# Performance work log

Measured on AMD Instinct MI355X. Metric: run time of the kernel, lower is better.

Reference implementation:

```python
import jax, jax.numpy as jnp
import numpy as np

N, E, D, EDIM = 50000, 800000, 128, 1
LN_EPS = 1e-5
NORM_FACTOR = 1.0


def _ln(x, g, b):
    m = jnp.mean(x, axis=-1, keepdims=True)
    v = jnp.var(x, axis=-1, keepdims=True)
    return (x - m) * jax.lax.rsqrt(v + LN_EPS) * g + b


def _mlp(x, w1, b1, g, be, w2, b2):
    # Linear -> SiLU -> LayerNorm -> Linear (matches nn.Sequential in msg_net/out_net)
    h = jax.nn.silu(x @ w1 + b1)
    h = _ln(h, g, be)
    return h @ w2 + b2


def setup_inputs() -> dict:
    key = jax.random.key(0)
    ks = jax.random.split(key, 24)
    s = 1.0 / np.sqrt(D)
    sa = 1.0 / np.sqrt(2 * D + EDIM)
    f32 = jnp.float32
    return {
        "h": jax.random.normal(ks[0], (N, D), f32),
        "edge_attr": jax.random.uniform(ks[1], (E, EDIM), f32),
        "row": jax.random.randint(ks[2], (E,), 0, N),
        "col": jax.random.randint(ks[3], (E,), 0, N),
        "node_mask": jnp.ones((N, 1), f32),
        "edge_mask": jnp.ones((E, 1), f32),
        "lin_w": jax.random.normal(ks[4], (D, D), f32) * s,
        "lin_b": jnp.zeros((D,), f32),
        "msg_w1": jax.random.normal(ks[5], (D, D), f32) * s,
        "msg_b1": jnp.zeros((D,), f32),
        "msg_ln_g": jnp.ones((D,), f32),
        "msg_ln_b": jnp.zeros((D,), f32),
        "msg_w2": jax.random.normal(ks[6], (D, D), f32) * s,
        "msg_b2": jnp.zeros((D,), f32),
        "att_w1": jax.random.normal(ks[7], (2 * D + EDIM, D), f32) * sa,
        "att_b1": jnp.zeros((D,), f32),
        "att_w2": jax.random.normal(ks[8], (D, 1), f32) * s,
        "att_b2": jnp.zeros((1,), f32),
        "out_w1": jax.random.normal(ks[9], (D, D), f32) * s,
        "out_b1": jnp.zeros((D,), f32),
        "out_ln_g": jnp.ones((D,), f32),
        "out_ln_b": jnp.zeros((D,), f32),
        "out_w2": jax.random.normal(ks[10], (D, D), f32) * s,
        "out_b2": jnp.zeros((D,), f32),
        "ln_g": jnp.ones((D,), f32),
        "ln_b": jnp.zeros((D,), f32),
    }


def reference(h, edge_attr, row, col, node_mask, edge_mask,
              lin_w, lin_b,
              msg_w1, msg_b1, msg_ln_g, msg_ln_b, msg_w2, msg_b2,
              att_w1, att_b1, att_w2, att_b2,
              out_w1, out_b1, out_ln_g, out_ln_b, out_w2, out_b2,
              ln_g, ln_b):
    # h = self.linear(h)
    x = h @ lin_w + lin_b                                    # [N, D]
    # msg_net transform of node features
    x_ = _mlp(x, msg_w1, msg_b1, msg_ln_g, msg_ln_b, msg_w2, msg_b2)
    # DenseAtt: cat(x[row], x[col], edge_attr) -> MLP -> sigmoid -> * edge_mask
    feat = jnp.concatenate([x[row], x[col], edge_attr], axis=1)   # [E, 2D+edge_dim]
    att = jax.nn.sigmoid(jax.nn.silu(feat @ att_w1 + att_b1) @ att_w2 + att_b2)
    att = att * edge_mask                                    # [E, 1]
    # gather -> weighted message -> scatter_add (unsorted_segment_sum, 'sum' norm)
    msg = jax.ops.segment_sum(x_[col] * att, row, num_segments=N) / NORM_FACTOR
    # out_net transform, residual, final LayerNorm
    msg = _mlp(msg, out_w1, out_b1, out_ln_g, out_ln_b, out_w2, out_b2)
    return _ln(x + msg, ln_g, ln_b)                          # [N, D]
```

## Files before the change

kernel.cpp:

```cpp
#include <hip/hip_runtime.h>

#define LN_EPS 1e-5f

typedef __attribute__((ext_vector_type(8))) short short8;
typedef __attribute__((ext_vector_type(4))) float f32x4;

__device__ __forceinline__ float sigf(float x) {
    return __builtin_amdgcn_rcpf(1.0f + __expf(-x));
}

__device__ __forceinline__ unsigned short f2bf(float f) {
    unsigned u = __float_as_uint(f);
    return (unsigned short)((u + 0x7fffu + ((u >> 16) & 1u)) >> 16);
}
__device__ __forceinline__ unsigned f2bf2(float lo, float hi) {
    return (unsigned)f2bf(lo) | ((unsigned)f2bf(hi) << 16);
}
__device__ __forceinline__ void bf2f(unsigned u, float& lo, float& hi) {
    lo = __uint_as_float(u << 16);
    hi = __uint_as_float(u & 0xffff0000u);
}
__device__ __forceinline__ void bf8f(uint4 p, float* o) {
    bf2f(p.x, o[0], o[1]); bf2f(p.y, o[2], o[3]);
    bf2f(p.z, o[4], o[5]); bf2f(p.w, o[6], o[7]);
}
__device__ __forceinline__ float bf1f(unsigned short s) {
    return __uint_as_float(((unsigned)s) << 16);
}

__device__ __forceinline__ float quad_add_all(float x) {
    int v = __builtin_amdgcn_update_dpp(0, __float_as_int(x), 0xB1, 0xF, 0xF, true);
    x += __int_as_float(v);
    v = __builtin_amdgcn_update_dpp(0, __float_as_int(x), 0x4E, 0xF, 0xF, true);
    x += __int_as_float(v);
    return x;
}

__global__ __launch_bounds__(256)
void prep_w(const float* __restrict__ lin_w, const float* __restrict__ msg_w1,
            const float* __restrict__ msg_w2, const float* __restrict__ att_w1,
            const float* __restrict__ out_w1, const float* __restrict__ out_w2,
            const float* __restrict__ att_b1, unsigned short* __restrict__ wp,
            float* __restrict__ bias256)
{
    const int idx = blockIdx.x * 256 + threadIdx.x;
    if (idx < 8 * 16384) {
        const int m = idx >> 14, r = idx & 16383;
        const int k = r >> 7, n = r & 127;
        const float* src; int slot; int fnBase = 0;
        switch (m) {
            case 0: src = lin_w;  slot = 0; break;
            case 1: src = msg_w1; slot = 1; break;
            case 2: src = msg_w2; slot = 2; break;
            case 3: src = att_w1; slot = 3; break;
            case 4: src = att_w1 + 128 * 128; slot = 3; fnBase = 8; break;
            case 5: src = out_w1; slot = 5; break;
            default: src = out_w2; slot = 6; break;
        }
        const float v = src[k * 128 + n];
        const int fn = fnBase + (n >> 4);
        const int fk = k >> 5, kb = (k >> 3) & 3, j = k & 7;
        const size_t dst = (size_t)slot * 16384 + ((size_t)((fn * 4 + fk) * 64 + (n & 15) + 16 * kb)) * 8 + j;
        wp[dst] = f2bf(v);
    } else if (idx < 8 * 16384 + 256) {
        const int t = idx - 8 * 16384;
        bias256[t] = (t < 128) ? att_b1[t] : 0.f;
    }
}

__device__ __forceinline__ short8 ldA_bf(const unsigned short* A, size_t row, int k0) {
    return *(const short8*)(A + row * 128 + k0);
}
__device__ __forceinline__ short8 ldA_f32(const float* A, size_t row, int k0) {
    const float* ap = A + row * 128 + k0;
    const float4 f0 = *(const float4*)ap;
    const float4 f1 = *(const float4*)(ap + 4);
    union { unsigned u[4]; short8 s; } v;
    v.u[0] = f2bf2(f0.x, f0.y); v.u[1] = f2bf2(f0.z, f0.w);
    v.u[2] = f2bf2(f1.x, f1.y); v.u[3] = f2bf2(f1.z, f1.w);
    return v.s;
}

template<int NFN, int ABF, int SPLIT>
__global__ __launch_bounds__(256, NFN == 8 ? 4 : 3)
void gemm_mfma(const void* __restrict__ Av, const unsigned short* __restrict__ Wp,
               const float* __restrict__ bias,
               unsigned short* __restrict__ C1, int ld1,
               unsigned short* __restrict__ C2, int ld2, int nrows)
{
    const int tid = threadIdx.x;
    const int w = tid >> 6, lane = tid & 63;
    const int r0 = blockIdx.x * 64;
    const int arow = r0 + w * 16 + (lane & 15);
    const size_t rowc = (arow < nrows) ? (size_t)arow : (size_t)(nrows - 1);
    const int kh = (lane >> 4) * 8;

    short8 a[4];
#pragma unroll
    for (int fk = 0; fk < 4; ++fk)
        a[fk] = ABF ? ldA_bf((const unsigned short*)Av, rowc, fk * 32 + kh)
                    : ldA_f32((const float*)Av, rowc, fk * 32 + kh);

    const short8* Bf = (const short8*)Wp;
    f32x4 acc[NFN];
#pragma unroll
    for (int fn = 0; fn < NFN; ++fn) acc[fn] = (f32x4){0.f, 0.f, 0.f, 0.f};
#pragma unroll
    for (int fk = 0; fk < 4; ++fk)
#pragma unroll
        for (int fn = 0; fn < NFN; ++fn)
            acc[fn] = __builtin_amdgcn_mfma_f32_16x16x32_bf16(a[fk], Bf[(fn * 4 + fk) * 64 + lane], acc[fn], 0, 0, 0);

    const int cn = lane & 15, rq = lane >> 4;
    float bv[NFN];
#pragma unroll
    for (int fn = 0; fn < NFN; ++fn) bv[fn] = bias ? bias[fn * 16 + cn] : 0.f;

#pragma unroll
    for (int reg = 0; reg < 4; ++reg) {
        const int gr = r0 + w * 16 + rq * 4 + reg;
        if (gr < nrows) {
#pragma unroll
            for (int fn = 0; fn < NFN; ++fn) {
                const float v = acc[fn][reg] + bv[fn];
                if (SPLIT) {
                    if (fn < 8) C1[(size_t)gr * ld1 + fn * 16 + cn] = f2bf(v);
                    else        C2[(size_t)gr * ld2 + (fn - 8) * 16 + cn] = f2bf(v);
                } else {
                    C1[(size_t)gr * ld1 + fn * 16 + cn] = f2bf(v);
                }
            }
        }
    }
}

template<int EPI2>
__global__ __launch_bounds__(256, 4)
void gemm2_mfma(const unsigned short* __restrict__ Av,
                const unsigned short* __restrict__ Wp1, const float* __restrict__ b1,
                const float* __restrict__ ln1g, const float* __restrict__ ln1b,
                const unsigned short* __restrict__ Wp2, const float* __restrict__ b2,
                const float* __restrict__ ln2g, const float* __restrict__ ln2b,
                const unsigned short* __restrict__ resH, void* __restrict__ Cv, int nrows)
{
    __shared__ unsigned short hof[4 * 2048];
    const int tid = threadIdx.x;
    const int w = tid >> 6, lane = tid & 63;
    const int r0 = blockIdx.x * 64;
    const int arow = r0 + w * 16 + (lane & 15);
    const size_t rowc = (arow < nrows) ? (size_t)arow : (size_t)(nrows - 1);
    const int kh = (lane >> 4) * 8;
    const int cn = lane & 15, rq = lane >> 4;

    short8 a[4];
#pragma unroll
    for (int fk = 0; fk < 4; ++fk)
        a[fk] = ldA_bf(Av, rowc, fk * 32 + kh);

    const short8* B1f = (const short8*)Wp1;
    f32x4 acc[8];
#pragma unroll
    for (int fn = 0; fn < 8; ++fn) acc[fn] = (f32x4){0.f, 0.f, 0.f, 0.f};
#pragma unroll
    for (int fk = 0; fk < 4; ++fk)
#pragma unroll
        for (int fn = 0; fn < 8; ++fn)
            acc[fn] = __builtin_amdgcn_mfma_f32_16x16x32_bf16(a[fk], B1f[(fn * 4 + fk) * 64 + lane], acc[fn], 0, 0, 0);

    unsigned short* hw = hof + w * 2048;
    {
        float bv[8], gv[8], bbv[8];
#pragma unroll
        for (int fn = 0; fn < 8; ++fn) {
            bv[fn] = b1[fn * 16 + cn]; gv[fn] = ln1g[fn * 16 + cn]; bbv[fn] = ln1b[fn * 16 + cn];
        }
#pragma unroll
        for (int reg = 0; reg < 4; ++reg) {
            float val[8];
            float sum = 0.f, sq = 0.f;
#pragma unroll
            for (int fn = 0; fn < 8; ++fn) {
                float v = acc[fn][reg] + bv[fn];
                v = v * sigf(v);
                val[fn] = v; sum += v; sq += v * v;
            }
#pragma unroll
            for (int m = 1; m < 16; m <<= 1) { sum += __shfl_xor(sum, m); sq += __shfl_xor(sq, m); }
            const float mean = sum * (1.f / 128.f);
            const float var = sq * (1.f / 128.f) - mean * mean;
            const float rstd = rsqrtf(var + LN_EPS);
            const int row16 = rq * 4 + reg;
            const int sw = (row16 & 7) << 3;
#pragma unroll
            for (int fn = 0; fn < 8; ++fn) {
                const float o = (val[fn] - mean) * rstd * gv[fn] + bbv[fn];
                hw[row16 * 128 + ((fn * 16 + cn) ^ sw)] = f2bf(o);
            }
        }
    }

    short8 a2[4];
    {
        const int row16 = lane & 15;
        const int sw = (row16 & 7) << 3;
#pragma unroll
        for (int fk = 0; fk < 4; ++fk)
            a2[fk] = *(const short8*)(hw + row16 * 128 + ((fk * 32 + kh) ^ sw));
    }

    const short8* B2f = (const short8*)Wp2;
    f32x4 acc2[8];
#pragma unroll
    for (int fn = 0; fn < 8; ++fn) acc2[fn] = (f32x4){0.f, 0.f, 0.f, 0.f};
#pragma unroll
    for (int fk = 0; fk < 4; ++fk)
#pragma unroll
        for (int fn = 0; fn < 8; ++fn)
            acc2[fn] = __builtin_amdgcn_mfma_f32_16x16x32_bf16(a2[fk], B2f[(fn * 4 + fk) * 64 + lane], acc2[fn], 0, 0, 0);

    float bv2[8];
#pragma unroll
    for (int fn = 0; fn < 8; ++fn) bv2[fn] = b2[fn * 16 + cn];

    if (EPI2 == 0) {
        unsigned short* Ch = (unsigned short*)Cv;
#pragma unroll
        for (int reg = 0; reg < 4; ++reg) {
            const int gr = r0 + w * 16 + rq * 4 + reg;
            if (gr < nrows) {
#pragma unroll
                for (int fn = 0; fn < 8; ++fn)
                    Ch[(size_t)gr * 128 + fn * 16 + cn] = f2bf(acc2[fn][reg] + bv2[fn]);
            }
        }
    } else {
        float* Cf = (float*)Cv;
        float gv[8], bbv[8];
#pragma unroll
        for (int fn = 0; fn < 8; ++fn) { gv[fn] = ln2g[fn * 16 + cn]; bbv[fn] = ln2b[fn * 16 + cn]; }
#pragma unroll
        for (int reg = 0; reg < 4; ++reg) {
            const int gr = r0 + w * 16 + rq * 4 + reg;
            const int grc = gr < nrows ? gr : nrows - 1;
            float val[8];
            float sum = 0.f, sq = 0.f;
#pragma unroll
            for (int fn = 0; fn < 8; ++fn) {
                float v = acc2[fn][reg] + bv2[fn] + bf1f(resH[(size_t)grc * 128 + fn * 16 + cn]);
                val[fn] = v; sum += v; sq += v * v;
            }
#pragma unroll
            for (int m = 1; m < 16; m <<= 1) { sum += __shfl_xor(sum, m); sq += __shfl_xor(sq, m); }
            const float mean = sum * (1.f / 128.f);
            const float var = sq * (1.f / 128.f) - mean * mean;
            const float rstd = rsqrtf(var + LN_EPS);
            if (gr < nrows) {
#pragma unroll
                for (int fn = 0; fn < 8; ++fn)
                    Cf[(size_t)gr * 128 + fn * 16 + cn] = (val[fn] - mean) * rstd * gv[fn] + bbv[fn];
            }
        }
    }
}


__global__ __launch_bounds__(256)
void hist_k(const int* __restrict__ row, int* __restrict__ cnt, int E)
{
    for (int e = blockIdx.x * blockDim.x + threadIdx.x; e < E; e += gridDim.x * blockDim.x)
        atomicAdd(&cnt[row[e]], 1);
}

__global__ __launch_bounds__(1024)
void scan_a(const int* __restrict__ cnt, int* __restrict__ off,
            int* __restrict__ btot, int n)
{
    __shared__ int wsum[16];
    const int tid = threadIdx.x, lane = tid & 63, wv = tid >> 6;
    const int i = blockIdx.x * 1024 + tid;
    const int v = (i < n) ? cnt[i] : 0;
    int incl = v;
#pragma unroll
    for (int d = 1; d < 64; d <<= 1) { int t = __shfl_up(incl, d); if (lane >= d) incl += t; }
    if (lane == 63) wsum[wv] = incl;
    __syncthreads();
    if (tid == 0) {
        int run = 0;
        for (int ww = 0; ww < 16; ++ww) { int t = wsum[ww]; wsum[ww] = run; run += t; }
    }
    __syncthreads();
    if (i < n) off[i] = wsum[wv] + incl - v;
    if (tid == 1023) btot[blockIdx.x] = wsum[15] + incl;
}

__global__ __launch_bounds__(64)
void scan_b(int* __restrict__ btot, int* __restrict__ bexc,
            int* __restrict__ off, int n, int nb, int E)
{
    const int t = threadIdx.x;
    const int v = (t < nb) ? btot[t] : 0;
    int incl = v;
#pragma unroll
    for (int d = 1; d < 64; d <<= 1) { int u = __shfl_up(incl, d); if (t >= d) incl += u; }
    if (t < nb) bexc[t] = incl - v;
    if (t == 0) off[n] = E;
}

__global__ __launch_bounds__(1024)
void scan_c(int* __restrict__ off, const int* __restrict__ bexc,
            int* __restrict__ cursor, int n)
{
    const int i = blockIdx.x * 1024 + threadIdx.x;
    if (i < n) {
        const int o = off[i] + bexc[blockIdx.x];
        off[i] = o;
        cursor[i] = o;
    }
}

__global__ __launch_bounds__(256)
void scatter_k(const int* __restrict__ row, const int* __restrict__ col,
               const float* __restrict__ ea, const float* __restrict__ em,
               int* __restrict__ cursor, uint4* __restrict__ erec, int E)
{
    const int tid = blockIdx.x * blockDim.x + threadIdx.x;
    const int stride = gridDim.x * blockDim.x;
    for (int e0 = tid; e0 < E; e0 += stride * 4) {
        uint4 rec[4]; int pos[4]; bool val[4];
#pragma unroll
        for (int u = 0; u < 4; ++u) {
            const int e = e0 + u * stride;
            val[u] = e < E;
            const int ec = val[u] ? e : 0;
            rec[u].x = (unsigned)row[ec];
            rec[u].y = (unsigned)col[ec];
            rec[u].z = __float_as_uint(ea[ec]);
            rec[u].w = __float_as_uint(em[ec]);
        }
#pragma unroll
        for (int u = 0; u < 4; ++u)
            if (val[u]) pos[u] = atomicAdd(&cursor[rec[u].x], 1);
#pragma unroll
        for (int u = 0; u < 4; ++u)
            if (val[u]) erec[pos[u]] = rec[u];
    }
}

__global__ __launch_bounds__(256, 4)
void att_edge(const unsigned short* __restrict__ xrH,
              const unsigned short* __restrict__ xcH,
              const uint4* __restrict__ erec, const float* __restrict__ we_,
              const float* __restrict__ w2_, const float* __restrict__ b2p,
              uint2* __restrict__ catS, int E)
{
    const int lane = threadIdx.x & 63;
    const int q = lane & 3;
    const int gwid = (blockIdx.x * blockDim.x + threadIdx.x) >> 6;
    const int nw = (gridDim.x * blockDim.x) >> 6;

    float we[32], w2[32];
#pragma unroll
    for (int ch = 0; ch < 4; ++ch) {
        const float4 a0 = ((const float4*)we_)[ch * 8 + q * 2];
        const float4 a1 = ((const float4*)we_)[ch * 8 + q * 2 + 1];
        we[ch * 8 + 0] = a0.x; we[ch * 8 + 1] = a0.y; we[ch * 8 + 2] = a0.z; we[ch * 8 + 3] = a0.w;
        we[ch * 8 + 4] = a1.x; we[ch * 8 + 5] = a1.y; we[ch * 8 + 6] = a1.z; we[ch * 8 + 7] = a1.w;
        const float4 c0 = ((const float4*)w2_)[ch * 8 + q * 2];
        const float4 c1 = ((const float4*)w2_)[ch * 8 + q * 2 + 1];
        w2[ch * 8 + 0] = c0.x; w2[ch * 8 + 1] = c0.y; w2[ch * 8 + 2] = c0.z; w2[ch * 8 + 3] = c0.w;
        w2[ch * 8 + 4] = c1.x; w2[ch * 8 + 5] = c1.y; w2[ch * 8 + 6] = c1.z; w2[ch * 8 + 7] = c1.w;
    }
    const float b2 = *b2p;

    for (int base = gwid * 16; base < E; base += nw * 16) {
        const int e = base + (lane >> 2);
        const bool valid = e < E;
        const int ec = valid ? e : E - 1;
        const uint4 rec = erec[ec];
        const int r = (int)rec.x, c = (int)rec.y;
        const float eax = __uint_as_float(rec.z);
        const float emv = __uint_as_float(rec.w);
        const unsigned short* xr = xrH + (size_t)r * 128;
        const unsigned short* xc = xcH + (size_t)c * 128;
        float p = 0.f;
#pragma unroll
        for (int ch = 0; ch < 4; ++ch) {
            const uint4 pa = *(const uint4*)(xr + ch * 32 + q * 8);
            const uint4 pb = *(const uint4*)(xc + ch * 32 + q * 8);
            float xa[8], xb[8];
            bf8f(pa, xa); bf8f(pb, xb);
#pragma unroll
            for (int i = 0; i < 8; ++i) {
                const float t = xa[i] + xb[i] + eax * we[ch * 8 + i];
                p += t * sigf(t) * w2[ch * 8 + i];
            }
        }
        p = quad_add_all(p);
        const float att = sigf(p + b2) * emv;
        if (valid && q == 0) catS[e] = make_uint2(rec.y, __float_as_uint(att));
    }
}

__global__ __launch_bounds__(256)
void accum_k(const unsigned short* __restrict__ xmH, const int* __restrict__ off,
             const uint2* __restrict__ catS, unsigned short* __restrict__ msgH, int N)
{
    const int lane = threadIdx.x & 63;
    const int g = lane >> 4, l = lane & 15;
    const int gwid = (blockIdx.x * blockDim.x + threadIdx.x) >> 6;
    const int nw = (gridDim.x * blockDim.x) >> 6;
    const uint4* xm4 = (const uint4*)xmH;

    for (int wid = gwid; wid < N; wid += nw) {
        int j0 = off[wid];
        const int jend = off[wid + 1];
        float acc[8] = {0.f, 0.f, 0.f, 0.f, 0.f, 0.f, 0.f, 0.f};

        for (; j0 + 16 <= jend; j0 += 16) {
            uint2 ca[4]; uint4 pk[4];
#pragma unroll
            for (int u = 0; u < 4; ++u) ca[u] = catS[j0 + u * 4 + g];
#pragma unroll
            for (int u = 0; u < 4; ++u) pk[u] = xm4[(size_t)ca[u].x * 16 + l];
#pragma unroll
            for (int u = 0; u < 4; ++u) {
                const float att = __uint_as_float(ca[u].y);
                float xm[8];
                bf8f(pk[u], xm);
#pragma unroll
                for (int i = 0; i < 8; ++i) acc[i] = fmaf(att, xm[i], acc[i]);
            }
        }
        for (; j0 + 8 <= jend; j0 += 8) {
            const uint2 caA = catS[j0 + g];
            const uint2 caB = catS[j0 + 4 + g];
            const uint4 pA = xm4[(size_t)caA.x * 16 + l];
            const uint4 pB = xm4[(size_t)caB.x * 16 + l];
            const float attA = __uint_as_float(caA.y);
            const float attB = __uint_as_float(caB.y);
            float xmA[8], xmB[8];
            bf8f(pA, xmA); bf8f(pB, xmB);
#pragma unroll
            for (int i = 0; i < 8; ++i)
                acc[i] = fmaf(attB, xmB[i], fmaf(attA, xmA[i], acc[i]));
        }
        for (; j0 < jend; j0 += 4) {
            const int je = j0 + g;
            const bool valid = je < jend;
            const int jc = valid ? je : jend - 1;
            const uint2 ca = catS[jc];
            const uint4 p = xm4[(size_t)ca.x * 16 + l];
            const float att = valid ? __uint_as_float(ca.y) : 0.f;
            float xm[8];
            bf8f(p, xm);
#pragma unroll
            for (int i = 0; i < 8; ++i) acc[i] = fmaf(att, xm[i], acc[i]);
        }

#pragma unroll
        for (int i = 0; i < 8; ++i) {
            acc[i] += __shfl_xor(acc[i], 16);
            acc[i] += __shfl_xor(acc[i], 32);
        }
        if (g == 0) {
            uint4 pk;
            pk.x = f2bf2(acc[0], acc[1]); pk.y = f2bf2(acc[2], acc[3]);
            pk.z = f2bf2(acc[4], acc[5]); pk.w = f2bf2(acc[6], acc[7]);
            ((uint4*)msgH)[(size_t)wid * 16 + l] = pk;
        }
    }
}

extern "C" void kernel_launch(void* const* d_in, const int* in_sizes, int n_in,
                              void* d_out, int out_size, void* d_ws, size_t ws_size,
                              hipStream_t stream)
{
    const float* h        = (const float*)d_in[0];
    const float* edge_attr= (const float*)d_in[1];
    const int*   row      = (const int*)d_in[2];
    const int*   col      = (const int*)d_in[3];
    const float* edge_mask= (const float*)d_in[5];
    const float* lin_w    = (const float*)d_in[6];
    const float* lin_b    = (const float*)d_in[7];
    const float* msg_w1   = (const float*)d_in[8];
    const float* msg_b1   = (const float*)d_in[9];
    const float* msg_ln_g = (const float*)d_in[10];
    const float* msg_ln_b = (const float*)d_in[11];
    const float* msg_w2   = (const float*)d_in[12];
    const float* msg_b2   = (const float*)d_in[13];
    const float* att_w1   = (const float*)d_in[14];
    const float* att_b1   = (const float*)d_in[15];
    const float* att_w2   = (const float*)d_in[16];
    const float* att_b2   = (const float*)d_in[17];
    const float* out_w1   = (const float*)d_in[18];
    const float* out_b1   = (const float*)d_in[19];
    const float* out_ln_g = (const float*)d_in[20];
    const float* out_ln_b = (const float*)d_in[21];
    const float* out_w2   = (const float*)d_in[22];
    const float* out_b2   = (const float*)d_in[23];
    const float* ln_g     = (const float*)d_in[24];
    const float* ln_b     = (const float*)d_in[25];

    const int N = in_sizes[0] / 128;
    const int E = in_sizes[2];
    const size_t NF = (size_t)N * 128;

    unsigned short* xbH  = (unsigned short*)d_ws;
    unsigned short* xrH  = xbH + NF;
    unsigned short* xcH  = xrH + NF;
    unsigned short* xmH  = xcH + NF;
    unsigned short* msgH = xmH + NF;
    int*    cnt   = (int*)(msgH + NF);
    int*    off   = cnt + N;
    int*    btot  = off + N + 8;
    int*    bexc  = btot + 64;
    uint4*  erec  = (uint4*)(bexc + 64 + 24);
    uint2*  catS  = (uint2*)(erec + E);
    unsigned short* wp = (unsigned short*)(catS + E);
    float* bias256 = (float*)(wp + 8 * 16384);

    const int gb = (N + 63) / 64;
    const int nb = (N + 1023) / 1024;
    const int sgrid = (E + 256 * 4 - 1) / (256 * 4);

    prep_w<<<513, 256, 0, stream>>>(lin_w, msg_w1, msg_w2, att_w1, out_w1, out_w2,
                                    att_b1, wp, bias256);
    hipMemsetAsync(cnt, 0, (size_t)N * sizeof(int), stream);
    hist_k<<<1024, 256, 0, stream>>>(row, cnt, E);
    scan_a<<<nb, 1024, 0, stream>>>(cnt, off, btot, N);
    scan_b<<<1, 64, 0, stream>>>(btot, bexc, off, N, nb, E);
    scan_c<<<nb, 1024, 0, stream>>>(off, bexc, cnt, N);
    scatter_k<<<sgrid, 256, 0, stream>>>(row, col, edge_attr, edge_mask,
                                         cnt, erec, E);

    gemm_mfma<8, 0, 0><<<gb, 256, 0, stream>>>(h, wp, lin_b, xbH, 128, nullptr, 0, N);
    gemm_mfma<16, 1, 1><<<gb, 256, 0, stream>>>(xbH, wp + 3 * 16384, bias256, xrH, 128, xcH, 128, N);
    att_edge<<<2048, 256, 0, stream>>>(xrH, xcH, erec,
                                       att_w1 + 256 * 128, att_w2, att_b2, catS, E);

    gemm2_mfma<0><<<gb, 256, 0, stream>>>(xbH, wp + 16384, msg_b1, msg_ln_g, msg_ln_b,
                                          wp + 2 * 16384, msg_b2, nullptr, nullptr,
                                          nullptr, xmH, N);

    accum_k<<<2048, 256, 0, stream>>>(xmH, off, catS, msgH, N);

    gemm2_mfma<3><<<gb, 256, 0, stream>>>(msgH, wp + 5 * 16384, out_b1, out_ln_g, out_ln_b,
                                          wp + 6 * 16384, out_b2, ln_g, ln_b,
                                          xbH, (float*)d_out, N);
}
```

Baseline: 249.1 us.

## Record per-edge rank in histogram and scatter attention results directly into CSR order

The histogram kernel now keeps the atomic return value as a per-edge rank. The separate scatter pass that built sorted 16-byte edge records is removed. The attention kernel reads row, col, edge_attr and edge_mask in original order and writes its (col, att) pair straight to off[row]+rank. This drops one kernel launch and an E-sized record write and read, at the cost of scattered 8-byte stores from att_edge and row-gather accesses in original edge order, which lose the row locality the sorted order gave.

```diff
diff --git a/kernel.cpp b/kernel.cpp
--- a/kernel.cpp
+++ b/kernel.cpp
@@ -263,12 +263,28 @@
     }
 }
 
-
 __global__ __launch_bounds__(256)
-void hist_k(const int* __restrict__ row, int* __restrict__ cnt, int E)
-{
-    for (int e = blockIdx.x * blockDim.x + threadIdx.x; e < E; e += gridDim.x * blockDim.x)
-        atomicAdd(&cnt[row[e]], 1);
+void hist_rank(const int* __restrict__ row, int* __restrict__ cnt,
+               int* __restrict__ rank, int E)
+{
+    const int tid = blockIdx.x * blockDim.x + threadIdx.x;
+    const int stride = gridDim.x * blockDim.x;
+    for (int e0 = tid; e0 < E; e0 += stride * 4) {
+        int r[4]; bool val[4];
+#pragma unroll
+        for (int u = 0; u < 4; ++u) {
+            const int e = e0 + u * stride;
+            val[u] = e < E;
+            r[u] = val[u] ? row[e] : 0;
+        }
+        int rk[4];
+#pragma unroll
+        for (int u = 0; u < 4; ++u)
+            if (val[u]) rk[u] = atomicAdd(&cnt[r[u]], 1);
+#pragma unroll
+        for (int u = 0; u < 4; ++u)
+            if (val[u]) rank[e0 + u * stride] = rk[u];
+    }
 }
 
 __global__ __launch_bounds__(1024)
@@ -307,51 +323,20 @@
 }
 
 __global__ __launch_bounds__(1024)
-void scan_c(int* __restrict__ off, const int* __restrict__ bexc,
-            int* __restrict__ cursor, int n)
+void scan_c(int* __restrict__ off, const int* __restrict__ bexc, int n)
 {
     const int i = blockIdx.x * 1024 + threadIdx.x;
-    if (i < n) {
-        const int o = off[i] + bexc[blockIdx.x];
-        off[i] = o;
-        cursor[i] = o;
-    }
-}
-
-__global__ __launch_bounds__(256)
-void scatter_k(const int* __restrict__ row, const int* __restrict__ col,
-               const float* __restrict__ ea, const float* __restrict__ em,
-               int* __restrict__ cursor, uint4* __restrict__ erec, int E)
-{
-    const int tid = blockIdx.x * blockDim.x + threadIdx.x;
-    const int stride = gridDim.x * blockDim.x;
-    for (int e0 = tid; e0 < E; e0 += stride * 4) {
-        uint4 rec[4]; int pos[4]; bool val[4];
-#pragma unroll
-        for (int u = 0; u < 4; ++u) {
-            const int e = e0 + u * stride;
-            val[u] = e < E;
-            const int ec = val[u] ? e : 0;
-            rec[u].x = (unsigned)row[ec];
-            rec[u].y = (unsigned)col[ec];
-            rec[u].z = __float_as_uint(ea[ec]);
-            rec[u].w = __float_as_uint(em[ec]);
-        }
-#pragma unroll
-        for (int u = 0; u < 4; ++u)
-            if (val[u]) pos[u] = atomicAdd(&cursor[rec[u].x], 1);
-#pragma unroll
-        for (int u = 0; u < 4; ++u)
-            if (val[u]) erec[pos[u]] = rec[u];
-    }
+    if (i < n) off[i] += bexc[blockIdx.x];
 }
 
 __global__ __launch_bounds__(256, 4)
 void att_edge(const unsigned short* __restrict__ xrH,
               const unsigned short* __restrict__ xcH,
-              const uint4* __restrict__ erec, const float* __restrict__ we_,
-              const float* __restrict__ w2_, const float* __restrict__ b2p,
-              uint2* __restrict__ catS, int E)
+              const int* __restrict__ row, const int* __restrict__ col,
+              const float* __restrict__ ea, const float* __restrict__ em,
+              const int* __restrict__ rank, const int* __restrict__ off,
+              const float* __restrict__ we_, const float* __restrict__ w2_,
+              const float* __restrict__ b2p, uint2* __restrict__ catS, int E)
 {
     const int lane = threadIdx.x & 63;
     const int q = lane & 3;
@@ -376,10 +361,8 @@
         const int e = base + (lane >> 2);
         const bool valid = e < E;
         const int ec = valid ? e : E - 1;
-        const uint4 rec = erec[ec];
-        const int r = (int)rec.x, c = (int)rec.y;
-        const float eax = __uint_as_float(rec.z);
-        const float emv = __uint_as_float(rec.w);
+        const int r = row[ec], c = col[ec];
+        const float eax = ea[ec], emv = em[ec];
         const unsigned short* xr = xrH + (size_t)r * 128;
         const unsigned short* xc = xcH + (size_t)c * 128;
         float p = 0.f;
@@ -397,7 +380,10 @@
         }
         p = quad_add_all(p);
         const float att = sigf(p + b2) * emv;
-        if (valid && q == 0) catS[e] = make_uint2(rec.y, __float_as_uint(att));
+        if (valid && q == 0) {
+            const int pos = off[r] + rank[ec];
+            catS[pos] = make_uint2((unsigned)c, __float_as_uint(att));
+        }
     }
 }
 
@@ -514,29 +500,28 @@
     int*    off   = cnt + N;
     int*    btot  = off + N + 8;
     int*    bexc  = btot + 64;
-    uint4*  erec  = (uint4*)(bexc + 64 + 24);
-    uint2*  catS  = (uint2*)(erec + E);
+    int*    rank  = bexc + 64;
+    uint2*  catS  = (uint2*)(rank + E);
     unsigned short* wp = (unsigned short*)(catS + E);
     float* bias256 = (float*)(wp + 8 * 16384);
 
     const int gb = (N + 63) / 64;
     const int nb = (N + 1023) / 1024;
-    const int sgrid = (E + 256 * 4 - 1) / (256 * 4);
+    const int hgrid = (E + 256 * 4 - 1) / (256 * 4);
 
     prep_w<<<513, 256, 0, stream>>>(lin_w, msg_w1, msg_w2, att_w1, out_w1, out_w2,
                                     att_b1, wp, bias256);
     hipMemsetAsync(cnt, 0, (size_t)N * sizeof(int), stream);
-    hist_k<<<1024, 256, 0, stream>>>(row, cnt, E);
+    hist_rank<<<hgrid, 256, 0, stream>>>(row, cnt, rank, E);
     scan_a<<<nb, 1024, 0, stream>>>(cnt, off, btot, N);
     scan_b<<<1, 64, 0, stream>>>(btot, bexc, off, N, nb, E);
-    scan_c<<<nb, 1024, 0, stream>>>(off, bexc, cnt, N);
-    scatter_k<<<sgrid, 256, 0, stream>>>(row, col, edge_attr, edge_mask,
-                                         cnt, erec, E);
+    scan_c<<<nb, 1024, 0, stream>>>(off, bexc, N);
 
     gemm_mfma<8, 0, 0><<<gb, 256, 0, stream>>>(h, wp, lin_b, xbH, 128, nullptr, 0, N);
     gemm_mfma<16, 1, 1><<<gb, 256, 0, stream>>>(xbH, wp + 3 * 16384, bias256, xrH, 128, xcH, 128, N);
-    att_edge<<<2048, 256, 0, stream>>>(xrH, xcH, erec,
-                                       att_w1 + 256 * 128, att_w2, att_b2, catS, E);
+    att_edge<<<2048, 256, 0, stream>>>(xrH, xcH, row, col, edge_attr, edge_mask,
+                                       rank, off, att_w1 + 256 * 128, att_w2, att_b2,
+                                       catS, E);
 
     gemm2_mfma<0><<<gb, 256, 0, stream>>>(xbH, wp + 16384, msg_b1, msg_ln_g, msg_ln_b,
                                           wp + 2 * 16384, msg_b2, nullptr, nullptr,
```

After: 231.5 us. 1.08x faster.
